# Kernel tuning notes

Measured on AMD Instinct MI355X. Metric: run time of the kernel, lower is better.

## Reference

```python
import jax, jax.numpy as jnp
import numpy as np

C = 64          # channels
K = 7           # 19 - 6*num with num=2 (conv_first, avg_pool, snake kernel size)
GN_GROUPS = C // 4


def conv2d(x, w, b=None, pad=(0, 0), groups=1):
    out = jax.lax.conv_general_dilated(
        x, w, window_strides=(1, 1),
        padding=((pad[0], pad[0]), (pad[1], pad[1])),
        dimension_numbers=('NCHW', 'OIHW', 'NCHW'),
        feature_group_count=groups)
    if b is not None:
        out = out + b[None, :, None, None]
    return out


def avg_pool(x, k, pad):
    # torch AvgPool2d default count_include_pad=True -> always divide by k*k
    s = jax.lax.reduce_window(x, 0.0, jax.lax.add, (1, 1, k, k), (1, 1, 1, 1),
                              ((0, 0), (0, 0), (pad, pad), (pad, pad)))
    return s / float(k * k)


def bn_eval(x, g, b, m, v, eps):
    inv = g / jnp.sqrt(v + eps)
    return x * inv[None, :, None, None] + (b - m * inv)[None, :, None, None]


def group_norm(x, g, b, groups, eps=1e-5):
    B, Ch, H, W = x.shape
    xr = x.reshape(B, groups, Ch // groups, H, W)
    mu = xr.mean(axis=(2, 3, 4), keepdims=True)
    var = xr.var(axis=(2, 3, 4), keepdims=True)
    xr = (xr - mu) / jnp.sqrt(var + eps)
    return xr.reshape(B, Ch, H, W) * g[None, :, None, None] + b[None, :, None, None]


def cum_offset(off):
    # Faithful to DSCNet DSC: center point pinned to 0, offsets accumulate outward
    # via `for index in range(1, center)`. The two endpoints keep their RAW,
    # DETACHED offsets (original code's off-by-one quirk on the detached clone).
    k = off.shape[1]
    c = k // 2
    new = [None] * k
    new[c] = jnp.zeros_like(off[:, c])
    for i in range(1, c):
        new[c + i] = new[c + i - 1] + off[:, c + i]
        new[c - i] = new[c - i + 1] + off[:, c - i]
    new[0] = jax.lax.stop_gradient(off[:, 0])
    new[k - 1] = jax.lax.stop_gradient(off[:, k - 1])
    return jnp.stack(new, axis=1)


def bilinear(feat, y, x):
    # feat [B,C,R,Cc]; y,x [B,K,R,Cc] -> samples [B,C,K,R,Cc]
    B, Ch, R, Cc = feat.shape
    y0 = jnp.floor(y)
    x0 = jnp.floor(x)
    y0i = jnp.clip(y0.astype(jnp.int32), 0, R - 1)
    y1i = jnp.clip(y0.astype(jnp.int32) + 1, 0, R - 1)
    x0i = jnp.clip(x0.astype(jnp.int32), 0, Cc - 1)
    x1i = jnp.clip(x0.astype(jnp.int32) + 1, 0, Cc - 1)
    gather = jax.vmap(lambda f, yi, xi: f[:, yi, xi])  # [C,R,Cc],[K,R,Cc]->[C,K,R,Cc]
    va0 = gather(feat, y0i, x0i)
    vc0 = gather(feat, y0i, x1i)
    va1 = gather(feat, y1i, x0i)
    vc1 = gather(feat, y1i, x1i)
    # interpolation weights use coords clamped to [0, max+1] (faithful to original)
    y0f = jnp.clip(y0, 0.0, float(R))
    y1f = jnp.clip(y0 + 1.0, 0.0, float(R))
    x0f = jnp.clip(x0, 0.0, float(Cc))
    x1f = jnp.clip(x0 + 1.0, 0.0, float(Cc))
    wa0 = ((y1f - y) * (x1f - x))[:, None]
    wc0 = ((y1f - y) * (x - x0f))[:, None]
    wa1 = ((y - y0f) * (x1f - x))[:, None]
    wc1 = ((y - y0f) * (x - x0f))[:, None]
    return va0 * wa0 + vc0 * wc0 + va1 * wa1 + vc1 * wc1


def dsconv(x, off_w, off_b, bn_g, bn_b, bn_m, bn_v, dsc_w, dsc_b, gn_g, gn_b, morph):
    # Dynamic Snake Conv (extend_scope=1, if_offset=True)
    B, Ch, R, Cc = x.shape
    off = jnp.tanh(bn_eval(conv2d(x, off_w, off_b, (1, 1)), bn_g, bn_b, bn_m, bn_v, 1e-5))
    y_off, x_off = off[:, :K], off[:, K:]
    spread = (jnp.arange(K, dtype=x.dtype) - K // 2)[None, :, None, None]
    rows = jnp.arange(R, dtype=x.dtype)[None, None, :, None]
    cols = jnp.arange(Cc, dtype=x.dtype)[None, None, None, :]
    if morph == 0:  # kernel spreads along x, snake swings in y
        y = rows + cum_offset(y_off)
        xc = cols + spread
    else:           # kernel spreads along y, snake swings in x
        y = rows + spread
        xc = cols + cum_offset(x_off)
    y = jnp.broadcast_to(y, (B, K, R, Cc))
    xc = jnp.broadcast_to(xc, (B, K, R, Cc))
    samp = bilinear(x, y, xc)  # [B,C,K,R,Cc]
    # strided (K,1)/(1,K) conv over the deformed map == contraction over (in, k)
    out = jnp.einsum('oik,bikrc->borc', dsc_w, samp) + dsc_b[None, :, None, None]
    out = group_norm(out, gn_g, gn_b, GN_GROUPS)
    return jax.nn.relu(out)


def setup_inputs() -> dict:
    key = jax.random.key(0)
    kit = iter(jax.random.split(key, 64))

    def rn(shape):
        if len(shape) == 1:
            return jax.random.normal(next(kit), shape, jnp.float32) * 0.05
        fan_in = int(np.prod(shape[1:]))
        return jax.random.normal(next(kit), shape, jnp.float32) / np.sqrt(fan_in)

    B, H, W = 2, 192, 192
    d = {}
    d['x'] = jax.random.normal(next(kit), (B, C, H, W), jnp.float32)
    d['w_first'] = rn((C, C, K, K))
    d['hc1_w'] = rn((C, 1, 1, 9)); d['hc1_b'] = rn((C,))
    d['hc2_w'] = rn((C, 1, 1, 7)); d['hc2_b'] = rn((C,))
    d['hc3_w'] = rn((C, 1, 1, 5)); d['hc3_b'] = rn((C,))
    d['vc1_w'] = rn((C, 1, 9, 1)); d['vc1_b'] = rn((C,))
    d['vc2_w'] = rn((C, 1, 7, 1)); d['vc2_b'] = rn((C,))
    d['vc3_w'] = rn((C, 1, 5, 1)); d['vc3_b'] = rn((C,))
    for p in ('h', 'v'):
        d[p + '_off_w'] = rn((2 * K, C, 3, 3)); d[p + '_off_b'] = rn((2 * K,))
        d[p + '_bn_g'] = 1.0 + rn((2 * K,)); d[p + '_bn_b'] = rn((2 * K,))
        d[p + '_bn_m'] = rn((2 * K,))
        d[p + '_bn_v'] = jax.random.uniform(next(kit), (2 * K,), jnp.float32) + 0.5
        d[p + '_dsc_w'] = rn((C, C, K)); d[p + '_dsc_b'] = rn((C,))
        d[p + '_gn_g'] = 1.0 + rn((C,)); d[p + '_gn_b'] = rn((C,))
    d['last_w'] = rn((C, C, 1, 1))
    d['last_g'] = 1.0 + rn((C,)); d['last_b'] = rn((C,))
    d['last_m'] = rn((C,))
    d['last_v'] = jax.random.uniform(next(kit), (C,), jnp.float32) + 0.5
    return d


def reference(x, w_first, hc1_w, hc1_b, hc2_w, hc2_b, hc3_w, hc3_b,
              vc1_w, vc1_b, vc2_w, vc2_b, vc3_w, vc3_b,
              h_off_w, h_off_b, h_bn_g, h_bn_b, h_bn_m, h_bn_v,
              h_dsc_w, h_dsc_b, h_gn_g, h_gn_b,
              v_off_w, v_off_b, v_bn_g, v_bn_b, v_bn_m, v_bn_v,
              v_dsc_w, v_dsc_b, v_gn_g, v_gn_b,
              last_w, last_g, last_b, last_m, last_v):
    x1 = avg_pool(conv2d(x, w_first, None, (K // 2, K // 2)), K, K // 2)
    h = conv2d(x1, hc1_w, hc1_b, (0, 4), groups=C)
    h = conv2d(h, hc2_w, hc2_b, (0, 3), groups=C)
    h = conv2d(h, hc3_w, hc3_b, (0, 2), groups=C)
    h = dsconv(h, h_off_w, h_off_b, h_bn_g, h_bn_b, h_bn_m, h_bn_v,
               h_dsc_w, h_dsc_b, h_gn_g, h_gn_b, morph=0)
    v = conv2d(x1, vc1_w, vc1_b, (4, 0), groups=C)
    v = conv2d(v, vc2_w, vc2_b, (3, 0), groups=C)
    v = conv2d(v, vc3_w, vc3_b, (2, 0), groups=C)
    v = dsconv(v, v_off_w, v_off_b, v_bn_g, v_bn_b, v_bn_m, v_bn_v,
               v_dsc_w, v_dsc_b, v_gn_g, v_gn_b, morph=1)
    out = h + v + x1
    out = conv2d(out, last_w, None, (0, 0))          # 1x1, bias=False (norm present)
    out = bn_eval(out, last_g, last_b, last_m, last_v, 1e-3)
    return out * jax.nn.sigmoid(out)                  # SiLU
```

## Files before the change

kernel.cpp:

```cpp
#include <hip/hip_runtime.h>
#include <hip/hip_bf16.h>
#include <hip/hip_fp16.h>
#include <math.h>

#define Bq 2
#define Cq 64
#define Hq 192
#define Wq 192
#define HWq (Hq*Wq)
#define Nq ((size_t)Bq*Cq*HWq)

typedef __attribute__((ext_vector_type(8))) _Float16 f16x8;
typedef __attribute__((ext_vector_type(4))) float f32x4;

__device__ inline unsigned short h2us(__half h) {
  union { __half h; unsigned short u; } v; v.h = h; return v.u;
}

__global__ __launch_bounds__(256) void prep_all_kernel(
    const float* hc1_w, const float* hc1_b, const float* hc2_w, const float* hc2_b,
    const float* hc3_w, const float* hc3_b,
    const float* vc1_w, const float* vc1_b, const float* vc2_w, const float* vc2_b,
    const float* vc3_w, const float* vc3_b,
    const float* h_off_w, const float* h_off_b, const float* h_bn_g, const float* h_bn_b,
    const float* h_bn_m, const float* h_bn_v,
    const float* v_off_w, const float* v_off_b, const float* v_bn_g, const float* v_bn_b,
    const float* v_bn_m, const float* v_bn_v,
    const float* last_w, const float* last_g, const float* last_b, const float* last_m,
    const float* last_v,
    const float* __restrict__ w_first,
    const float* __restrict__ h_dsc_w, const float* __restrict__ v_dsc_w,
    float* wEffH, float* bEffH, float* wEffV, float* bEffV,
    float* wOffH, float* bOffH, float* wOffV, float* bOffV,
    float* lwT, float* lbO, float* wB,
    unsigned short* __restrict__ wtpH, unsigned short* __restrict__ wtpV,
    unsigned short* __restrict__ wpack)
{
  int bid = blockIdx.x;
  int t = threadIdx.x;
  if (bid == 0) {
    if (t < 128) {
      int ch = t & 63;
      bool ish = t < 64;
      const float* w1p = (ish ? hc1_w : vc1_w) + ch*9;
      const float* w2p = (ish ? hc2_w : vc2_w) + ch*7;
      const float* w3p = (ish ? hc3_w : vc3_w) + ch*5;
      float w1r[9], w2r[7], w3r[5];
#pragma unroll
      for (int j = 0; j < 9; j++) w1r[j] = w1p[j];
#pragma unroll
      for (int k = 0; k < 7; k++) w2r[k] = w2p[k];
#pragma unroll
      for (int m = 0; m < 5; m++) w3r[m] = w3p[m];
      float t15[15];
#pragma unroll
      for (int s = 0; s < 15; s++) {
        float a = 0.f;
#pragma unroll
        for (int j = 0; j < 9; j++) { int k2 = s - j; if (k2 >= 0 && k2 < 7) a += w1r[j]*w2r[k2]; }
        t15[s] = a;
      }
      float* we = (ish ? wEffH : wEffV) + ch*19;
#pragma unroll
      for (int s = 0; s < 19; s++) {
        float a = 0.f;
#pragma unroll
        for (int j = 0; j < 15; j++) { int k3 = s - j; if (k3 >= 0 && k3 < 5) a += t15[j]*w3r[k3]; }
        we[s] = a;
      }
      float S2 = 0.f, S3 = 0.f;
#pragma unroll
      for (int j = 0; j < 7; j++) S2 += w2r[j];
#pragma unroll
      for (int j = 0; j < 5; j++) S3 += w3r[j];
      float b1 = (ish ? hc1_b : vc1_b)[ch];
      float b2 = (ish ? hc2_b : vc2_b)[ch];
      float b3 = (ish ? hc3_b : vc3_b)[ch];
      (ish ? bEffH : bEffV)[ch] = b1*S2*S3 + b2*S3 + b3;
    }
    for (int idx = t; idx < 9*64*7; idx += 256) {
      int tap = idx / 448; int rem = idx % 448; int i = rem / 7; int m = rem % 7;
      float invh = h_bn_g[m] / sqrtf(h_bn_v[m] + 1e-5f);
      wOffH[(tap*64 + i)*8 + m] = h_off_w[(m*64 + i)*9 + tap] * invh;
      float invv = v_bn_g[7+m] / sqrtf(v_bn_v[7+m] + 1e-5f);
      wOffV[(tap*64 + i)*8 + m] = v_off_w[((7+m)*64 + i)*9 + tap] * invv;
    }
    if (t < 7) {
      float invh = h_bn_g[t] / sqrtf(h_bn_v[t] + 1e-5f);
      bOffH[t] = h_off_b[t]*invh + h_bn_b[t] - h_bn_m[t]*invh;
      float invv = v_bn_g[7+t] / sqrtf(v_bn_v[7+t] + 1e-5f);
      bOffV[t] = v_off_b[7+t]*invv + v_bn_b[7+t] - v_bn_m[7+t]*invv;
    }
    for (int idx = t; idx < 4096; idx += 256) {
      int o = idx % 64; int i = idx / 64;
      float inv = last_g[o] / sqrtf(last_v[o] + 1e-3f);
      lwT[i*64 + o] = last_w[o*64 + i] * inv;
    }
    if (t < 64) {
      float inv = last_g[t] / sqrtf(last_v[t] + 1e-3f);
      lbO[t] = last_b[t] - last_m[t]*inv;
    }
  } else if (bid <= 9) {
    int tid = (bid - 1)*256 + t;
    if (tid >= 2*64*18) return;
    int cls = tid % 18;
    int ch  = (tid / 18) % 64;
    int br  = tid / (18*64);
    int c = (cls < 9) ? cls : cls + 174;
    const float* w1p = (br==0 ? hc1_w : vc1_w) + ch*9;
    const float* w2p = (br==0 ? hc2_w : vc2_w) + ch*7;
    const float* w3p = (br==0 ? hc3_w : vc3_w) + ch*5;
    float b1 = (br==0 ? hc1_b : vc1_b)[ch];
    float b2 = (br==0 ? hc2_b : vc2_b)[ch];
    float b3 = (br==0 ? hc3_b : vc3_b)[ch];
    float w1r[9], w2r[7], w3r[5];
#pragma unroll
    for (int j = 0; j < 9; j++) w1r[j] = w1p[j];
#pragma unroll
    for (int k = 0; k < 7; k++) w2r[k] = w2p[k];
#pragma unroll
    for (int m = 0; m < 5; m++) w3r[m] = w3p[m];
    float acc[19];
#pragma unroll
    for (int s = 0; s < 19; s++) acc[s] = 0.f;
    float bacc = b3;
#pragma unroll
    for (int m = 0; m < 5; m++) {
      int d = c + m - 2;
      bool dok = (d >= 0 && d < Wq);
      float s2b = b2;
#pragma unroll
      for (int k = 0; k < 7; k++) {
        int e = d + k - 3;
        bool eok = (e >= 0 && e < Wq);
        if (eok) s2b += w2r[k] * b1;
        float wmk = w3r[m] * w2r[k];
#pragma unroll
        for (int j = 0; j < 9; j++) {
          int fd = e + j - 4;
          bool fok = (fd >= 0 && fd < Wq);
          float contrib = (dok && eok && fok) ? wmk * w1r[j] : 0.f;
          acc[m + k + j] += contrib;
        }
      }
      if (dok) bacc += w3r[m] * s2b;
    }
    float* dst = wB + ((size_t)(br*64 + ch)*18 + cls)*20;
#pragma unroll
    for (int s = 0; s < 19; s++) dst[s] = acc[s];
    dst[19] = bacc;
  } else {
    int tid = (bid - 10)*256 + t;
    int nthr = 64*256;
    for (int idx = tid; idx < 7*2*2*64*32; idx += nthr) {
      int ch32 = idx & 31;
      int oc   = (idx >> 5) & 63;
      int hl   = (idx >> 11) & 1;
      int kc   = (idx >> 12) & 1;
      int tap  = idx >> 13;
      int i = kc*32 + ch32;
      float vh = h_dsc_w[oc*448 + i*7 + tap];
      float vv = v_dsc_w[oc*448 + i*7 + tap];
      _Float16 hh = (_Float16)vh;
      _Float16 hv = (_Float16)vv;
      unsigned short uh, uv;
      if (!hl) { uh = *(unsigned short*)&hh; uv = *(unsigned short*)&hv; }
      else {
        _Float16 lh = (_Float16)(vh - (float)hh);
        _Float16 lv = (_Float16)(vv - (float)hv);
        uh = *(unsigned short*)&lh; uv = *(unsigned short*)&lv;
      }
      wtpH[idx] = uh; wtpV[idx] = uv;
    }
    for (int e = tid; e < 2*49*2*64*32; e += nthr) {
      int ch  = e & 31;
      int oc  = (e >> 5) & 63;
      int hl  = (e >> 11) & 1;
      int rest = e >> 12;
      int tap = rest % 49;
      int h   = rest / 49;
      float wv = w_first[((size_t)oc*64 + h*32 + ch)*49 + tap];
      __half hh = __float2half(wv);
      unsigned short us;
      if (!hl) us = h2us(hh);
      else { float rr = wv - __half2float(hh); us = h2us(__float2half(rr)); }
      wpack[e] = us;
    }
  }
}

__global__ __launch_bounds__(192) void tof16_pack_kernel(const float* __restrict__ x,
                                                         unsigned short* __restrict__ xpack)
{
  __shared__ unsigned int s[192*64];
  int r = blockIdx.x, b = blockIdx.y;
  int t = threadIdx.x;
  for (int ch = 0; ch < 64; ch++) {
    float v = x[((size_t)(b*64+ch)*Hq + r)*Wq + t];
    _Float16 hh = (_Float16)v;
    s[t*64 + (ch ^ (t & 31))] = (unsigned int)*(unsigned short*)&hh;
  }
  __syncthreads();
  unsigned short* dst = xpack + ((size_t)b*Hq + r)*Wq*64;
  for (int i = 0; i < 8; i++) {
    int gidx = i*192 + t;
    int c = gidx >> 3, g = gidx & 7;
    unsigned short tmp[8];
#pragma unroll
    for (int j = 0; j < 8; j++) {
      int ch = g*8 + j;
      tmp[j] = (unsigned short)s[c*64 + (ch ^ (c & 31))];
    }
    uint4 v;
    v.x = (unsigned int)tmp[0] | ((unsigned int)tmp[1] << 16);
    v.y = (unsigned int)tmp[2] | ((unsigned int)tmp[3] << 16);
    v.z = (unsigned int)tmp[4] | ((unsigned int)tmp[5] << 16);
    v.w = (unsigned int)tmp[6] | ((unsigned int)tmp[7] << 16);
    *(uint4*)(dst + (size_t)gidx*8) = v;
  }
}

__global__ __launch_bounds__(256) void conv7_mfma_kernel(
    const unsigned short* __restrict__ xpack,
    const unsigned short* __restrict__ wpack,
    float* __restrict__ out)
{
  __shared__ __align__(16) unsigned short sA[8*54*32];
  int ct = blockIdx.x;
  int rt = blockIdx.y;
  int b  = blockIdx.z;
  int r0 = rt*2, c0 = ct*48;
  int t = threadIdx.x;
  int wv = t >> 6;
  int l  = t & 63;
  int l15 = l & 15, lg = l >> 4;
  int oc = wv*16 + l15;

  f32x4 acc[2][3];
#pragma unroll
  for (int i = 0; i < 2; i++)
#pragma unroll
    for (int j = 0; j < 3; j++) acc[i][j] = (f32x4){0.f,0.f,0.f,0.f};

  for (int h = 0; h < 2; h++) {
    __syncthreads();
    for (int idx = t; idx < 8*54*4; idx += 256) {
      int g = idx & 3, pix = idx >> 2;
      int row = pix / 54, col = pix % 54;
      int gr = r0 - 3 + row, gc = c0 - 3 + col;
      uint4 v = {0u,0u,0u,0u};
      if (gr >= 0 && gr < Hq && gc >= 0 && gc < Wq)
        v = *(const uint4*)(xpack + (((size_t)b*Hq + gr)*Wq + gc)*64 + (h*4 + g)*8);
      ((uint4*)sA)[(row*54 + col)*4 + (g ^ ((col >> 1) & 3))] = v;
    }
    __syncthreads();
    const unsigned short* wb = wpack + (size_t)h*49*4096;
#pragma unroll 7
    for (int tap = 0; tap < 49; tap++) {
      int dy = tap / 7, dx = tap % 7;
      f16x8 bh = *(const f16x8*)(wb + (size_t)tap*4096 +        oc*32 + lg*8);
      f16x8 bl = *(const f16x8*)(wb + (size_t)tap*4096 + 2048 + oc*32 + lg*8);
#pragma unroll
      for (int rw = 0; rw < 2; rw++) {
        int arow = rw + dy;
        f16x8 a[3];
#pragma unroll
        for (int tc = 0; tc < 3; tc++) {
          int col = tc*16 + l15 + dx;
          a[tc] = *(const f16x8*)((const uint4*)sA + (arow*54 + col)*4 + (lg ^ ((col >> 1) & 3)));
        }
#pragma unroll
        for (int tc = 0; tc < 3; tc++) {
          acc[rw][tc] = __builtin_amdgcn_mfma_f32_16x16x32_f16(a[tc], bh, acc[rw][tc], 0, 0, 0);
          acc[rw][tc] = __builtin_amdgcn_mfma_f32_16x16x32_f16(a[tc], bl, acc[rw][tc], 0, 0, 0);
        }
      }
    }
  }
#pragma unroll
  for (int rw = 0; rw < 2; rw++) {
    float* dst = out + ((size_t)(b*64 + oc)*Hq + (r0 + rw))*Wq + c0;
#pragma unroll
    for (int tc = 0; tc < 3; tc++) {
      f32x4 v = acc[rw][tc];
      *(float4*)(dst + tc*16 + lg*4) = make_float4(v[0], v[1], v[2], v[3]);
    }
  }
}

__global__ __launch_bounds__(256) void pool_fused_kernel(const float* __restrict__ in,
                                                         float* __restrict__ out)
{
  __shared__ float raw[38][192];
  __shared__ float cs[32][192];
  int rt = blockIdx.x;
  int plane = blockIdx.y;
  int r0 = rt*32;
  int t = threadIdx.x;
  const float* src = in + (size_t)plane*HWq;
  for (int idx = t; idx < 38*192; idx += 256) {
    int lr = idx / 192, c = idx % 192;
    int gr = r0 - 3 + lr;
    raw[lr][c] = (gr >= 0 && gr < Hq) ? src[gr*Wq + c] : 0.f;
  }
  __syncthreads();
  for (int idx = t; idx < 32*192; idx += 256) {
    int lr = idx / 192, c = idx % 192;
    float s = 0.f;
#pragma unroll
    for (int dr = 0; dr < 7; dr++) s += raw[lr + dr][c];
    cs[lr][c] = s;
  }
  __syncthreads();
  float* dst = out + (size_t)plane*HWq + r0*Wq;
  for (int idx = t; idx < 32*192; idx += 256) {
    int lr = idx / 192, c = idx % 192;
    float s = 0.f;
#pragma unroll
    for (int dc = -3; dc <= 3; dc++) {
      int cc = c + dc;
      if (cc >= 0 && cc < Wq) s += cs[lr][cc];
    }
    dst[idx] = s * (1.f/49.f);
  }
}

__global__ __launch_bounds__(256) void dwf_kernel(const float* __restrict__ x1,
                                                  const float* __restrict__ wEffH,
                                                  const float* __restrict__ bEffH,
                                                  const float* __restrict__ wBH,
                                                  const float* __restrict__ wEffV,
                                                  const float* __restrict__ bEffV,
                                                  const float* __restrict__ wBV,
                                                  unsigned short* __restrict__ packH,
                                                  unsigned short* __restrict__ packV)
{
  __shared__ float sW[8][19][20];
  int z = blockIdx.z;
  int br = z >> 1, b = z & 1;
  const float* wEff = br ? wEffV : wEffH;
  const float* bEff = br ? bEffV : bEffH;
  const float* wB   = br ? wBV   : wBH;
  unsigned short* pack = br ? packV : packH;
  int g8 = blockIdx.y;
  int t = threadIdx.x;
  int chb = g8*8;
  for (int i = t; i < 8*380; i += 256) {
    int ch8 = i / 380; int rem = i % 380;
    int row = rem / 20, jj = rem % 20;
    int ch = chb + ch8;
    float v;
    if (row < 18) v = wB[((size_t)ch*18 + row)*20 + jj];
    else v = (jj < 19) ? wEff[ch*19 + jj] : bEff[ch];
    sW[ch8][row][jj] = v;
  }
  __syncthreads();
  int p = blockIdx.x*256 + t;
  int r = p / Wq, c = p % Wq;
  float vals[8];
  if (br == 0) {
    int row = (c < 9) ? c : ((c >= Wq-9) ? (c - 174) : 18);
#pragma unroll
    for (int ch8 = 0; ch8 < 8; ch8++) {
      const float* src = x1 + (size_t)(b*Cq + chb + ch8)*HWq + r*Wq;
      float s = sW[ch8][row][19];
#pragma unroll
      for (int j = 0; j < 19; j++) {
        int idx = min(max(c + j - 9, 0), Wq-1);
        s += src[idx] * sW[ch8][row][j];
      }
      vals[ch8] = s;
    }
  } else {
    int row = (r < 9) ? r : ((r >= Hq-9) ? (r - 174) : 18);
#pragma unroll
    for (int ch8 = 0; ch8 < 8; ch8++) {
      const float* src = x1 + (size_t)(b*Cq + chb + ch8)*HWq + c;
      float s = sW[ch8][row][19];
#pragma unroll
      for (int j = 0; j < 19; j++) {
        int idx = min(max(r + j - 9, 0), Hq-1);
        s += src[idx*Wq] * sW[ch8][row][j];
      }
      vals[ch8] = s;
    }
  }
  unsigned int hi[4], lo[4];
#pragma unroll
  for (int q = 0; q < 4; q++) {
    __half h0 = __float2half(vals[2*q]);
    __half h1 = __float2half(vals[2*q+1]);
    __half l0 = __float2half(vals[2*q]   - __half2float(h0));
    __half l1 = __float2half(vals[2*q+1] - __half2float(h1));
    hi[q] = (unsigned int)h2us(h0) | ((unsigned int)h2us(h1) << 16);
    lo[q] = (unsigned int)h2us(l0) | ((unsigned int)h2us(l1) << 16);
  }
  *(uint4*)(pack + (((size_t)b*16 + g8)*HWq + p)*8)     = make_uint4(hi[0], hi[1], hi[2], hi[3]);
  *(uint4*)(pack + (((size_t)b*16 + 8 + g8)*HWq + p)*8) = make_uint4(lo[0], lo[1], lo[2], lo[3]);
}

__global__ __launch_bounds__(256) void off_cum_kernel(const unsigned short* __restrict__ fpH,
                                                      const unsigned short* __restrict__ fpV,
                                                      const float* __restrict__ wOffH,
                                                      const float* __restrict__ bOffH,
                                                      const float* __restrict__ wOffV,
                                                      const float* __restrict__ bOffV,
                                                      float* __restrict__ hcum,
                                                      float* __restrict__ vcum)
{
  const size_t HW8 = (size_t)HWq*8;
  int bid = blockIdx.x;
  int xcd = bid & 7, lid = bid >> 3;
  int combo = xcd >> 1;
  int br = combo >> 1, b = combo & 1;
  int pxblk = (xcd & 1)*72 + lid;
  const unsigned short* fp = br ? fpV : fpH;
  const float* wOff = br ? wOffV : wOffH;
  const float* bOff = br ? bOffV : bOffH;
  float* cum = br ? vcum : hcum;
  int p = pxblk*256 + threadIdx.x;
  int r = p / Wq, c = p % Wq;
  float tv[7];
#pragma unroll
  for (int m = 0; m < 7; m++) tv[m] = bOff[m];
  const unsigned short* fb = fp + (size_t)b*HWq*128;
  for (int tap = 0; tap < 9; tap++) {
    int dy = tap/3 - 1, dx = tap%3 - 1;
    int rr = r + dy, cc = c + dx;
    if (rr < 0 || rr >= Hq || cc < 0 || cc >= Wq) continue;
    const unsigned short* p0 = fb + ((size_t)rr*Wq + cc)*8;
    const float* wp = wOff + tap*512;
    for (int g = 0; g < 8; g++) {
      f16x8 hv = *(const f16x8*)(p0 + (size_t)g*HW8);
      f16x8 lv = *(const f16x8*)(p0 + (size_t)(8 + g)*HW8);
#pragma unroll
      for (int e = 0; e < 8; e++) {
        float fv = (float)hv[e] + (float)lv[e];
        const float* wr = wp + (g*8 + e)*8;
#pragma unroll
        for (int m = 0; m < 7; m++) tv[m] += fv * wr[m];
      }
    }
  }
#pragma unroll
  for (int m = 0; m < 7; m++) tv[m] = tanhf(tv[m]);
  float c0 = tv[0], c1 = tv[1] + tv[2], c2 = tv[2], c3 = 0.f;
  float c4 = tv[4], c5 = tv[4] + tv[5], c6 = tv[6];
  size_t bb = (size_t)b*7*HWq + p;
  cum[bb + 0*HWq] = c0; cum[bb + 1*HWq] = c1; cum[bb + 2*HWq] = c2;
  cum[bb + 3*HWq] = c3; cum[bb + 4*HWq] = c4; cum[bb + 5*HWq] = c5;
  cum[bb + 6*HWq] = c6;
}

__global__ __launch_bounds__(64, 4) void einsum_mfma_kernel(
    const unsigned short* __restrict__ fpH, const unsigned short* __restrict__ fpV,
    const float* __restrict__ cumH, const float* __restrict__ cumV,
    const unsigned short* __restrict__ wtpHp, const unsigned short* __restrict__ wtpVp,
    const float* __restrict__ dscbH, const float* __restrict__ dscbV,
    float* __restrict__ outH, float* __restrict__ outV,
    float* __restrict__ pstat)
{
  __shared__ __align__(16) unsigned short sA[2*32*64];
  const size_t HW8 = (size_t)HWq*8;
  int morph = blockIdx.y;
  const unsigned short* fp  = morph ? fpV   : fpH;
  const float* cum          = morph ? cumV  : cumH;
  const unsigned short* wtp = morph ? wtpVp : wtpHp;
  const float* dsc_b        = morph ? dscbV : dscbH;
  float* out                = morph ? outV  : outH;
  int bid = blockIdx.x;
  int swz = (bid & 7)*288 + (bid >> 3);
  int b   = swz / 1152;
  int blk = swz % 1152;
  int l = threadIdx.x;
  int l15 = l & 15, lg = l >> 4;
  int l7 = l & 7;
  int px5 = l & 31;
  int chh = l >> 5;
  int p = blk*32 + px5;
  int r = p / Wq, c = p % Wq;

  f32x4 acc[2][4];
#pragma unroll
  for (int i = 0; i < 2; i++)
#pragma unroll
    for (int j = 0; j < 4; j++) acc[i][j] = (f32x4){0.f,0.f,0.f,0.f};

  const unsigned short* fb = fp + (size_t)b*HWq*128;

  for (int kp = 0; kp < 4; kp++) {
    int k0 = kp*2;
    int nk = (kp < 3) ? 2 : 1;
    for (int kk = 0; kk < nk; kk++) {
      int k = k0 + kk;
      unsigned short* myrow = sA + (size_t)(kk*32 + px5)*64;
      bool oob;
      const unsigned short *p0, *p1;
      float w0, w1;
      if (morph == 0) {
        int xi = c + k - 3;
        oob = (xi < 0 || xi >= Wq);
        if (!oob) {
          float y = (float)r + cum[((size_t)(b*7 + k))*HWq + p];
          float y0 = floorf(y);
          int y0q = (int)y0;
          int y0i = min(max(y0q, 0), Hq-1);
          int y1i = min(max(y0q + 1, 0), Hq-1);
          float y0f = fminf(fmaxf(y0, 0.f), (float)Hq);
          float y1f = fminf(fmaxf(y0 + 1.f, 0.f), (float)Hq);
          w0 = y1f - y; w1 = y - y0f;
          p0 = fb + ((size_t)y0i*Wq + xi)*8;
          p1 = fb + ((size_t)y1i*Wq + xi)*8;
        }
      } else {
        int yi = r + k - 3;
        oob = (yi < 0 || yi >= Hq);
        if (!oob) {
          float xf = (float)c + cum[((size_t)(b*7 + k))*HWq + p];
          float x0 = floorf(xf);
          int x0q = (int)x0;
          int x0i = min(max(x0q, 0), Wq-1);
          int x1i = min(max(x0q + 1, 0), Wq-1);
          float x0f = fminf(fmaxf(x0, 0.f), (float)Wq);
          float x1f = fminf(fmaxf(x0 + 1.f, 0.f), (float)Wq);
          w0 = x1f - xf; w1 = xf - x0f;
          p0 = fb + ((size_t)yi*Wq + x0i)*8;
          p1 = fb + ((size_t)yi*Wq + x1i)*8;
        }
      }
      if (oob) {
        uint4 z = {0u,0u,0u,0u};
#pragma unroll
        for (int gi = 0; gi < 4; gi++) {
          int g = chh*4 + gi;
          *(uint4*)(myrow + (size_t)(g ^ l7)*8) = z;
        }
      } else {
#pragma unroll
        for (int gi = 0; gi < 4; gi++) {
          int g = chh*4 + gi;
          f16x8 a0h = *(const f16x8*)(p0 + (size_t)g*HW8);
          f16x8 a1h = *(const f16x8*)(p1 + (size_t)g*HW8);
          f16x8 sh;
#pragma unroll
          for (int e = 0; e < 8; e++) {
            float v = w0*(float)a0h[e] + w1*(float)a1h[e];
            sh[e] = (_Float16)v;
          }
          *(f16x8*)(myrow + (size_t)(g ^ l7)*8) = sh;
        }
      }
    }
    for (int kk = 0; kk < nk; kk++) {
      int k = k0 + kk;
#pragma unroll
      for (int kc = 0; kc < 2; kc++) {
        const unsigned short* wbase = wtp + (size_t)((k*2 + kc)*2)*2048;
        f16x8 bh[4], bl[4];
#pragma unroll
        for (int tb = 0; tb < 4; tb++) {
          bh[tb] = *(const f16x8*)(wbase + (tb*16 + l15)*32 + lg*8);
          bl[tb] = *(const f16x8*)(wbase + 2048 + (tb*16 + l15)*32 + lg*8);
        }
        f16x8 ah[2];
#pragma unroll
        for (int ta = 0; ta < 2; ta++) {
          const unsigned short* rbase = sA + (size_t)(kk*32 + ta*16 + l15)*64;
          ah[ta] = *(const f16x8*)(rbase + (size_t)((kc*4 + lg) ^ l7)*8);
        }
#pragma unroll
        for (int ta = 0; ta < 2; ta++)
#pragma unroll
          for (int tb = 0; tb < 4; tb++) {
            acc[ta][tb] = __builtin_amdgcn_mfma_f32_16x16x32_f16(ah[ta], bh[tb], acc[ta][tb], 0, 0, 0);
            acc[ta][tb] = __builtin_amdgcn_mfma_f32_16x16x32_f16(ah[ta], bl[tb], acc[ta][tb], 0, 0, 0);
          }
      }
    }
  }
  int pbase = blk*32;
#pragma unroll
  for (int tb = 0; tb < 4; tb++) {
    int oc = tb*16 + l15;
    float bias = dsc_b[oc];
    float* dst = out + (size_t)(b*64 + oc)*HWq + pbase;
    float s = 0.f, ss = 0.f;
#pragma unroll
    for (int ta = 0; ta < 2; ta++) {
      f32x4 v = acc[ta][tb];
      float v0 = v[0]+bias, v1 = v[1]+bias, v2 = v[2]+bias, v3 = v[3]+bias;
      *(float4*)(dst + ta*16 + lg*4) = make_float4(v0, v1, v2, v3);
      s  += v0 + v1 + v2 + v3;
      ss += v0*v0 + v1*v1 + v2*v2 + v3*v3;
    }
    s  += __shfl_xor(s, 16);
    s  += __shfl_xor(s, 32);
    ss += __shfl_xor(ss, 16);
    ss += __shfl_xor(ss, 32);
    if (lg == 0) {
      float* pp = pstat + ((size_t)(morph*2304 + swz))*128 + oc*2;
      pp[0] = s; pp[1] = ss;
    }
  }
}

__global__ __launch_bounds__(256) void gnred_kernel(const float* __restrict__ pstat,
                                                    float* __restrict__ stats)
{
  int combo = blockIdx.x;
  int buf = combo >> 7;
  int rem = combo & 127;
  int b = rem >> 6, ch = rem & 63;
  int t = threadIdx.x;
  float s = 0.f, ss = 0.f;
  for (int q = t; q < 1152; q += 256) {
    const float* pp = pstat + ((size_t)(buf*2304 + b*1152 + q))*128 + ch*2;
    s += pp[0]; ss += pp[1];
  }
  __shared__ float red[2][4];
  for (int off = 32; off; off >>= 1) {
    s  += __shfl_down(s, off);
    ss += __shfl_down(ss, off);
  }
  if ((t & 63) == 0) { red[0][t >> 6] = s; red[1][t >> 6] = ss; }
  __syncthreads();
  if (t == 0) {
    s  = red[0][0] + red[0][1] + red[0][2] + red[0][3];
    ss = red[1][0] + red[1][1] + red[1][2] + red[1][3];
    stats[combo*2 + 0] = s;
    stats[combo*2 + 1] = ss;
  }
}

__global__ __launch_bounds__(256) void gnfinal_kernel(const float* __restrict__ stats,
                                                      const float* __restrict__ h_gn_g, const float* __restrict__ h_gn_b,
                                                      const float* __restrict__ v_gn_g, const float* __restrict__ v_gn_b,
                                                      float* __restrict__ gnAB)
{
  int t = threadIdx.x;
  int buf = t >> 7, ch = t & 63;
  int base = t & ~3;
  float sum = 0.f, ss = 0.f;
#pragma unroll
  for (int q = 0; q < 4; q++) { sum += stats[(base+q)*2]; ss += stats[(base+q)*2 + 1]; }
  const float n = 4.f * HWq;
  float mean = sum / n;
  float var = ss / n - mean*mean;
  float gg = (buf ? v_gn_g : h_gn_g)[ch];
  float bb = (buf ? v_gn_b : h_gn_b)[ch];
  float A = gg / sqrtf(var + 1e-5f);
  gnAB[t*2 + 0] = A;
  gnAB[t*2 + 1] = bb - mean*A;
}

__global__ __launch_bounds__(256) void final2_kernel(const float* __restrict__ hbuf,
                                                     const float* __restrict__ vbuf,
                                                     const float* __restrict__ x1,
                                                     const float* __restrict__ gnAB,
                                                     const float* __restrict__ lwT,
                                                     const float* __restrict__ lbO,
                                                     float* __restrict__ out)
{
  int b = blockIdx.y;
  int p = blockIdx.x*256 + threadIdx.x;
  float acc[64];
#pragma unroll
  for (int o = 0; o < 64; o++) acc[o] = 0.f;
  for (int i = 0; i < 64; i++) {
    size_t off = (size_t)(b*64 + i)*HWq + p;
    int plane = b*64 + i;
    int ih = plane*2;
    int iv = (128 + plane)*2;
    float hv = fmaxf(hbuf[off]*gnAB[ih] + gnAB[ih+1], 0.f);
    float vv = fmaxf(vbuf[off]*gnAB[iv] + gnAB[iv+1], 0.f);
    float cv = hv + vv + x1[off];
    const float* wr = lwT + i*64;
#pragma unroll
    for (int o = 0; o < 64; o++) acc[o] += cv * wr[o];
  }
  float* dst = out + (size_t)b*Cq*HWq + p;
#pragma unroll
  for (int o = 0; o < 64; o++) {
    float yv = acc[o] + lbO[o];
    dst[(size_t)o*HWq] = yv / (1.f + expf(-yv));
  }
}

extern "C" void kernel_launch(void* const* d_in, const int* in_sizes, int n_in,
                              void* d_out, int out_size, void* d_ws, size_t ws_size,
                              hipStream_t stream)
{
  const float* x       = (const float*)d_in[0];
  const float* w_first = (const float*)d_in[1];
  float* ws = (float*)d_ws;

  float* bufA = ws;
  float* bufB = ws + Nq;
  float* x1   = ws + 2*Nq;
  float* h_ds = ws + 3*Nq;
  float* v_ds = ws + 4*Nq;
  size_t off = 5*Nq;
  float* hcum  = ws + off; off += (size_t)Bq*7*HWq;
  float* vcum  = ws + off; off += (size_t)Bq*7*HWq;
  float* wEffH = ws + off; off += 64*19;
  float* bEffH = ws + off; off += 64;
  float* wEffV = ws + off; off += 64*19;
  float* bEffV = ws + off; off += 64;
  float* wtH   = ws + off; off += 64*64*7;
  float* wtV   = ws + off; off += 64*64*7;
  float* wOffH = ws + off; off += 9*64*8;
  float* bOffH = ws + off; off += 8;
  float* wOffV = ws + off; off += 9*64*8;
  float* bOffV = ws + off; off += 8;
  float* lwT   = ws + off; off += 64*64;
  float* lbO   = ws + off; off += 64;
  float* stats = ws + off; off += 512;
  float* gnAB  = ws + off; off += 512;
  float* wB    = ws + off; off += 2*64*18*20;
  float* pstat = ws + off; off += (size_t)2*2304*128;
  unsigned short* wpack = (unsigned short*)(ws + off); off += 2*49*2*64*32/2 + 16;
  unsigned short* xpack  = (unsigned short*)h_ds;
  unsigned short* fpackH = (unsigned short*)h_ds;
  unsigned short* fpackV = (unsigned short*)v_ds;
  unsigned short* wtpH = (unsigned short*)wtH;
  unsigned short* wtpV = (unsigned short*)wtV;

  prep_all_kernel<<<dim3(74), dim3(256), 0, stream>>>(
      (const float*)d_in[2],  (const float*)d_in[3],  (const float*)d_in[4],  (const float*)d_in[5],
      (const float*)d_in[6],  (const float*)d_in[7],
      (const float*)d_in[8],  (const float*)d_in[9],  (const float*)d_in[10], (const float*)d_in[11],
      (const float*)d_in[12], (const float*)d_in[13],
      (const float*)d_in[14], (const float*)d_in[15], (const float*)d_in[16], (const float*)d_in[17],
      (const float*)d_in[18], (const float*)d_in[19],
      (const float*)d_in[24], (const float*)d_in[25], (const float*)d_in[26], (const float*)d_in[27],
      (const float*)d_in[28], (const float*)d_in[29],
      (const float*)d_in[34], (const float*)d_in[35], (const float*)d_in[36], (const float*)d_in[37],
      (const float*)d_in[38],
      w_first, (const float*)d_in[20], (const float*)d_in[30],
      wEffH, bEffH, wEffV, bEffV, wOffH, bOffH, wOffV, bOffV, lwT, lbO, wB,
      wtpH, wtpV, wpack);

  tof16_pack_kernel<<<dim3(Hq, Bq), dim3(192), 0, stream>>>(x, xpack);
  conv7_mfma_kernel<<<dim3(4, 96, 2), dim3(256), 0, stream>>>(xpack, wpack, bufA);

  pool_fused_kernel<<<dim3(6, 128), dim3(256), 0, stream>>>(bufA, x1);

  dwf_kernel<<<dim3(144, 8, 4), dim3(256), 0, stream>>>(x1, wEffH, bEffH, wB,
      wEffV, bEffV, wB + 64*18*20, fpackH, fpackV);

  off_cum_kernel<<<dim3(576), dim3(256), 0, stream>>>(fpackH, fpackV,
      wOffH, bOffH, wOffV, bOffV, hcum, vcum);

  einsum_mfma_kernel<<<dim3(2304, 2), dim3(64), 0, stream>>>(fpackH, fpackV,
      hcum, vcum, wtpH, wtpV, (const float*)d_in[21], (const float*)d_in[31], bufA, bufB, pstat);

  gnred_kernel<<<dim3(256), dim3(256), 0, stream>>>(pstat, stats);
  gnfinal_kernel<<<dim3(1), dim3(256), 0, stream>>>(stats,
      (const float*)d_in[22], (const float*)d_in[23],
      (const float*)d_in[32], (const float*)d_in[33], gnAB);

  final2_kernel<<<dim3(144, 2), dim3(256), 0, stream>>>(bufA, bufB, x1, gnAB, lwT, lbO, (float*)d_out);
}
```

Before: 306.8 us.

## Software-pipeline einsum bilinear gathers and enlarge conv7 row tile to three rows

The einsum kernel now issues the gathers for the next tap into registers before running the MFMAs for the current tap, writing the interpolated samples into a double-buffered LDS slot afterward. This is meant to hide global load latency behind matrix work. The occupancy hint drops from 4 to 3 waves to leave registers for the prefetched data. The conv7 kernel now computes three output rows per block instead of two, which cuts halo reloads and launches fewer blocks but uses more accumulators and LDS.

New measurement: 302.7 us. No clear change (-1.3%).

```diff
diff --git a/kernel.cpp b/kernel.cpp
--- a/kernel.cpp
+++ b/kernel.cpp
@@ -225,26 +225,26 @@
     const unsigned short* __restrict__ wpack,
     float* __restrict__ out)
 {
-  __shared__ __align__(16) unsigned short sA[8*54*32];
+  __shared__ __align__(16) unsigned short sA[9*54*32];
   int ct = blockIdx.x;
   int rt = blockIdx.y;
   int b  = blockIdx.z;
-  int r0 = rt*2, c0 = ct*48;
+  int r0 = rt*3, c0 = ct*48;
   int t = threadIdx.x;
   int wv = t >> 6;
   int l  = t & 63;
   int l15 = l & 15, lg = l >> 4;
   int oc = wv*16 + l15;
 
-  f32x4 acc[2][3];
-#pragma unroll
-  for (int i = 0; i < 2; i++)
+  f32x4 acc[3][3];
+#pragma unroll
+  for (int i = 0; i < 3; i++)
 #pragma unroll
     for (int j = 0; j < 3; j++) acc[i][j] = (f32x4){0.f,0.f,0.f,0.f};
 
   for (int h = 0; h < 2; h++) {
     __syncthreads();
-    for (int idx = t; idx < 8*54*4; idx += 256) {
+    for (int idx = t; idx < 9*54*4; idx += 256) {
       int g = idx & 3, pix = idx >> 2;
       int row = pix / 54, col = pix % 54;
       int gr = r0 - 3 + row, gc = c0 - 3 + col;
@@ -261,7 +261,7 @@
       f16x8 bh = *(const f16x8*)(wb + (size_t)tap*4096 +        oc*32 + lg*8);
       f16x8 bl = *(const f16x8*)(wb + (size_t)tap*4096 + 2048 + oc*32 + lg*8);
 #pragma unroll
-      for (int rw = 0; rw < 2; rw++) {
+      for (int rw = 0; rw < 3; rw++) {
         int arow = rw + dy;
         f16x8 a[3];
 #pragma unroll
@@ -278,7 +278,7 @@
     }
   }
 #pragma unroll
-  for (int rw = 0; rw < 2; rw++) {
+  for (int rw = 0; rw < 3; rw++) {
     float* dst = out + ((size_t)(b*64 + oc)*Hq + (r0 + rw))*Wq + c0;
 #pragma unroll
     for (int tc = 0; tc < 3; tc++) {
@@ -452,7 +452,7 @@
   cum[bb + 6*HWq] = c6;
 }
 
-__global__ __launch_bounds__(64, 4) void einsum_mfma_kernel(
+__global__ __launch_bounds__(64, 3) void einsum_mfma_kernel(
     const unsigned short* __restrict__ fpH, const unsigned short* __restrict__ fpV,
     const float* __restrict__ cumH, const float* __restrict__ cumV,
     const unsigned short* __restrict__ wtpHp, const unsigned short* __restrict__ wtpVp,
@@ -480,6 +480,10 @@
   int p = blk*32 + px5;
   int r = p / Wq, c = p % Wq;
 
+  int fixc   = morph ? r : c;
+  int vbase  = morph ? c : r;
+  int stride = morph ? 1 : Wq;
+
   f32x4 acc[2][4];
 #pragma unroll
   for (int i = 0; i < 2; i++)
@@ -488,96 +492,97 @@
 
   const unsigned short* fb = fp + (size_t)b*HWq*128;
 
-  for (int kp = 0; kp < 4; kp++) {
-    int k0 = kp*2;
-    int nk = (kp < 3) ? 2 : 1;
-    for (int kk = 0; kk < nk; kk++) {
-      int k = k0 + kk;
-      unsigned short* myrow = sA + (size_t)(kk*32 + px5)*64;
-      bool oob;
-      const unsigned short *p0, *p1;
-      float w0, w1;
-      if (morph == 0) {
-        int xi = c + k - 3;
-        oob = (xi < 0 || xi >= Wq);
-        if (!oob) {
-          float y = (float)r + cum[((size_t)(b*7 + k))*HWq + p];
-          float y0 = floorf(y);
-          int y0q = (int)y0;
-          int y0i = min(max(y0q, 0), Hq-1);
-          int y1i = min(max(y0q + 1, 0), Hq-1);
-          float y0f = fminf(fmaxf(y0, 0.f), (float)Hq);
-          float y1f = fminf(fmaxf(y0 + 1.f, 0.f), (float)Hq);
-          w0 = y1f - y; w1 = y - y0f;
-          p0 = fb + ((size_t)y0i*Wq + xi)*8;
-          p1 = fb + ((size_t)y1i*Wq + xi)*8;
-        }
-      } else {
-        int yi = r + k - 3;
-        oob = (yi < 0 || yi >= Hq);
-        if (!oob) {
-          float xf = (float)c + cum[((size_t)(b*7 + k))*HWq + p];
-          float x0 = floorf(xf);
-          int x0q = (int)x0;
-          int x0i = min(max(x0q, 0), Wq-1);
-          int x1i = min(max(x0q + 1, 0), Wq-1);
-          float x0f = fminf(fmaxf(x0, 0.f), (float)Wq);
-          float x1f = fminf(fmaxf(x0 + 1.f, 0.f), (float)Wq);
-          w0 = x1f - xf; w1 = xf - x0f;
-          p0 = fb + ((size_t)yi*Wq + x0i)*8;
-          p1 = fb + ((size_t)yi*Wq + x1i)*8;
-        }
-      }
-      if (oob) {
-        uint4 z = {0u,0u,0u,0u};
-#pragma unroll
-        for (int gi = 0; gi < 4; gi++) {
-          int g = chh*4 + gi;
-          *(uint4*)(myrow + (size_t)(g ^ l7)*8) = z;
-        }
-      } else {
-#pragma unroll
-        for (int gi = 0; gi < 4; gi++) {
-          int g = chh*4 + gi;
-          f16x8 a0h = *(const f16x8*)(p0 + (size_t)g*HW8);
-          f16x8 a1h = *(const f16x8*)(p1 + (size_t)g*HW8);
-          f16x8 sh;
-#pragma unroll
-          for (int e = 0; e < 8; e++) {
-            float v = w0*(float)a0h[e] + w1*(float)a1h[e];
-            sh[e] = (_Float16)v;
-          }
-          *(f16x8*)(myrow + (size_t)(g ^ l7)*8) = sh;
-        }
-      }
-    }
-    for (int kk = 0; kk < nk; kk++) {
-      int k = k0 + kk;
-#pragma unroll
-      for (int kc = 0; kc < 2; kc++) {
-        const unsigned short* wbase = wtp + (size_t)((k*2 + kc)*2)*2048;
-        f16x8 bh[4], bl[4];
-#pragma unroll
-        for (int tb = 0; tb < 4; tb++) {
-          bh[tb] = *(const f16x8*)(wbase + (tb*16 + l15)*32 + lg*8);
-          bl[tb] = *(const f16x8*)(wbase + 2048 + (tb*16 + l15)*32 + lg*8);
-        }
-        f16x8 ah[2];
-#pragma unroll
-        for (int ta = 0; ta < 2; ta++) {
-          const unsigned short* rbase = sA + (size_t)(kk*32 + ta*16 + l15)*64;
-          ah[ta] = *(const f16x8*)(rbase + (size_t)((kc*4 + lg) ^ l7)*8);
-        }
-#pragma unroll
-        for (int ta = 0; ta < 2; ta++)
-#pragma unroll
-          for (int tb = 0; tb < 4; tb++) {
-            acc[ta][tb] = __builtin_amdgcn_mfma_f32_16x16x32_f16(ah[ta], bh[tb], acc[ta][tb], 0, 0, 0);
-            acc[ta][tb] = __builtin_amdgcn_mfma_f32_16x16x32_f16(ah[ta], bl[tb], acc[ta][tb], 0, 0, 0);
-          }
-      }
-    }
-  }
+  f16x8 a0r[4], a1r[4];
+  float w0, w1;
+  bool oob;
+
+#define ISSUE(KK)                                                           \
+  {                                                                         \
+    int fx = fixc + (KK) - 3;                                               \
+    oob = (fx < 0 || fx >= 192);                                            \
+    float vf = (float)vbase + cum[((size_t)(b*7 + (KK)))*HWq + p];          \
+    float v0 = floorf(vf);                                                  \
+    int v0q = (int)v0;                                                      \
+    int v0i = min(max(v0q, 0), 191);                                        \
+    int v1i = min(max(v0q + 1, 0), 191);                                    \
+    float v0f = fminf(fmaxf(v0, 0.f), 192.f);                               \
+    float v1f = fminf(fmaxf(v0 + 1.f, 0.f), 192.f);                         \
+    w0 = v1f - vf; w1 = vf - v0f;                                           \
+    int fixoff = morph ? fx*Wq : fx;                                        \
+    const unsigned short* p0 = fb + (size_t)(fixoff + v0i*stride)*8;        \
+    const unsigned short* p1 = fb + (size_t)(fixoff + v1i*stride)*8;        \
+    if (!oob) {                                                             \
+      _Pragma("unroll")                                                     \
+      for (int gi = 0; gi < 4; gi++) {                                      \
+        int g = chh*4 + gi;                                                 \
+        a0r[gi] = *(const f16x8*)(p0 + (size_t)g*HW8);                      \
+        a1r[gi] = *(const f16x8*)(p1 + (size_t)g*HW8);                      \
+      }                                                                     \
+    }                                                                       \
+  }
+
+#define WRITE(SLOT)                                                         \
+  {                                                                         \
+    unsigned short* myrow = sA + (size_t)((SLOT)*32 + px5)*64;              \
+    if (oob) {                                                              \
+      uint4 z = {0u,0u,0u,0u};                                              \
+      _Pragma("unroll")                                                     \
+      for (int gi = 0; gi < 4; gi++)                                        \
+        *(uint4*)(myrow + (size_t)(((chh*4 + gi) ^ l7))*8) = z;             \
+    } else {                                                                \
+      _Pragma("unroll")                                                     \
+      for (int gi = 0; gi < 4; gi++) {                                      \
+        f16x8 sh;                                                           \
+        _Pragma("unroll")                                                   \
+        for (int e = 0; e < 8; e++) {                                       \
+          float v = w0*(float)a0r[gi][e] + w1*(float)a1r[gi][e];            \
+          sh[e] = (_Float16)v;                                              \
+        }                                                                   \
+        *(f16x8*)(myrow + (size_t)(((chh*4 + gi) ^ l7))*8) = sh;            \
+      }                                                                     \
+    }                                                                       \
+  }
+
+#define MFMA_TAP(KK, SLOT)                                                  \
+  {                                                                         \
+    _Pragma("unroll")                                                       \
+    for (int kc = 0; kc < 2; kc++) {                                        \
+      const unsigned short* wbase = wtp + (size_t)(((KK)*2 + kc)*2)*2048;   \
+      f16x8 bh[4], bl[4];                                                   \
+      _Pragma("unroll")                                                     \
+      for (int tb = 0; tb < 4; tb++) {                                      \
+        bh[tb] = *(const f16x8*)(wbase + (tb*16 + l15)*32 + lg*8);          \
+        bl[tb] = *(const f16x8*)(wbase + 2048 + (tb*16 + l15)*32 + lg*8);   \
+      }                                                                     \
+      f16x8 ah[2];                                                          \
+      _Pragma("unroll")                                                     \
+      for (int ta = 0; ta < 2; ta++) {                                      \
+        const unsigned short* rbase = sA + (size_t)((SLOT)*32 + ta*16 + l15)*64; \
+        ah[ta] = *(const f16x8*)(rbase + (size_t)((kc*4 + lg) ^ l7)*8);     \
+      }                                                                     \
+      _Pragma("unroll")                                                     \
+      for (int ta = 0; ta < 2; ta++)                                        \
+        _Pragma("unroll")                                                   \
+        for (int tb = 0; tb < 4; tb++) {                                    \
+          acc[ta][tb] = __builtin_amdgcn_mfma_f32_16x16x32_f16(ah[ta], bh[tb], acc[ta][tb], 0, 0, 0); \
+          acc[ta][tb] = __builtin_amdgcn_mfma_f32_16x16x32_f16(ah[ta], bl[tb], acc[ta][tb], 0, 0, 0); \
+        }                                                                   \
+    }                                                                       \
+  }
+
+  ISSUE(0);
+  WRITE(0);
+#pragma unroll 1
+  for (int k = 0; k < 7; k++) {
+    int slot = k & 1;
+    if (k < 6) ISSUE(k+1);
+    MFMA_TAP(k, slot);
+    if (k < 6) WRITE((k+1) & 1);
+  }
+#undef ISSUE
+#undef WRITE
+#undef MFMA_TAP
+
   int pbase = blk*32;
 #pragma unroll
   for (int tb = 0; tb < 4; tb++) {
@@ -741,7 +746,7 @@
       wtpH, wtpV, wpack);
 
   tof16_pack_kernel<<<dim3(Hq, Bq), dim3(192), 0, stream>>>(x, xpack);
-  conv7_mfma_kernel<<<dim3(4, 96, 2), dim3(256), 0, stream>>>(xpack, wpack, bufA);
+  conv7_mfma_kernel<<<dim3(4, 64, 2), dim3(256), 0, stream>>>(xpack, wpack, bufA);
 
   pool_fused_kernel<<<dim3(6, 128), dim3(256), 0, stream>>>(bufA, x1);
 
```
